# Optimization experiments

Hardware: AMD Instinct MI355X
Metric: run time of the kernel (lower is better)

The kernel has to match this reference:

```python
import jax, jax.numpy as jnp
import numpy as np

B, T, P, D = 8, 512, 2048, 768
TOKEN_HALF = 0.15
PATCH_HALF = 0.03  # small patch boxes


def _make_boxes(key, b, n, half):
    c = jax.random.uniform(key, (b, n, 2), dtype=jnp.float32)
    lo = jnp.clip(c - half, 0.0, 1.0)
    hi = jnp.clip(c + half, 0.0, 1.0)
    return jnp.concatenate([lo, hi], axis=-1)  # (b, n, 4): x0,y0,x1,y1


def setup_inputs() -> dict:
    key = jax.random.key(0)
    k1, k2, k3, k4 = jax.random.split(key, 4)
    patch_feats = jax.random.normal(k1, (B, P, D), dtype=jnp.float32)
    token_boxes = _make_boxes(k2, B, T, TOKEN_HALF)
    patch_boxes = _make_boxes(k3, B, P, PATCH_HALF)
    token_mask = jnp.ones((B, T), dtype=bool)
    scorer_w = jax.random.normal(k4, (D,), dtype=jnp.float32) * 0.02
    scorer_b = jnp.zeros((1,), dtype=jnp.float32)
    return {"patch_feats": patch_feats, "token_boxes": token_boxes,
            "patch_boxes": patch_boxes, "token_mask": token_mask,
            "scorer_w": scorer_w, "scorer_b": scorer_b}


def _patches_in_token_boxes(patch_boxes, tb):
    # patch center containment test: (B,T,P) bool
    cx = 0.5 * (patch_boxes[..., 0] + patch_boxes[..., 2])  # (B,P)
    cy = 0.5 * (patch_boxes[..., 1] + patch_boxes[..., 3])  # (B,P)
    cx = cx[:, None, :]
    cy = cy[:, None, :]
    return ((cx >= tb[..., 0:1]) & (cx <= tb[..., 2:3]) &
            (cy >= tb[..., 1:2]) & (cy <= tb[..., 3:4]))


def reference(patch_feats, token_boxes, patch_boxes, token_mask, scorer_w, scorer_b):
    # normalize token boxes if given in 0..1000 coords (data-dependent, via where)
    tb = token_boxes
    scale = jnp.where(tb.max() > 1.5, jnp.float32(1.0 / 1000.0), jnp.float32(1.0))
    tb = tb * scale

    in_box = _patches_in_token_boxes(patch_boxes, tb)          # (B,T,P)
    in_box = in_box & token_mask[:, :, None]
    region_mask = jnp.any(in_box, axis=-1)                      # (B,T)

    scores = patch_feats @ scorer_w + scorer_b[0]               # (B,P)
    scores = jnp.broadcast_to(scores[:, None, :], in_box.shape)  # (B,T,P)
    scores = jnp.where(in_box, scores, jnp.float32(-10000.0))
    attn = jax.nn.softmax(scores, axis=-1)                      # (B,T,P)

    region_feats = jnp.einsum('btp,bpd->btd', attn, patch_feats)
    region_feats = region_feats * region_mask[..., None].astype(region_feats.dtype)
    return region_feats, region_mask
```

## Files before the change

### kernel.cpp

```cpp
#include <hip/hip_runtime.h>

#define B 8
#define T 512
#define P 2048
#define D 768
#define KDIM P
#define NSPLIT 4
#define KSPLIT (KDIM / NSPLIT)

typedef unsigned short ushort_t;
using short8 = __attribute__((ext_vector_type(8))) short;
using f32x4v = __attribute__((ext_vector_type(4))) float;

#define IDX_SCALE 0
#define IDX_SCORES 64
#define IDX_SCORES2 (64 + B*P)
#define IDX_CX (64 + B*P)
#define IDX_CY (64 + 2*B*P)
#define OFF_ATTN_BYTES 197120
#define OFF_FT_BYTES (OFF_ATTN_BYTES + (size_t)B*T*P*2)
#define OFF_PART_BYTES (OFF_FT_BYTES + (size_t)B*D*P*2)
#define WS_NEED (OFF_PART_BYTES + (size_t)NSPLIT*B*T*D*4)

#define GLD16(gsrc, ldst) \
    __builtin_amdgcn_global_load_lds((const __attribute__((address_space(1))) void*)(gsrc), \
                                     (__attribute__((address_space(3))) void*)(ldst), 16, 0, 0)

__device__ inline ushort_t f2bf(float x) {
    union { float f; unsigned u; } v; v.f = x;
    unsigned r = v.u + 0x7fffu + ((v.u >> 16) & 1u);
    return (ushort_t)(r >> 16);
}

__global__ void k_scale(const float* __restrict__ tboxes, float* __restrict__ ws) {
    __shared__ float red[4];
    int tid = threadIdx.x;
    float m = -1e30f;
    const float4* tb4 = (const float4*)tboxes;
    #pragma unroll
    for (int i = 0; i < 16; ++i) {
        float4 v = tb4[tid + i * 256];
        m = fmaxf(fmaxf(fmaxf(m, v.x), fmaxf(v.y, v.z)), v.w);
    }
    #pragma unroll
    for (int off = 1; off < 64; off <<= 1) m = fmaxf(m, __shfl_xor(m, off));
    if ((tid & 63) == 0) red[tid >> 6] = m;
    __syncthreads();
    if (tid == 0) {
        float mb = fmaxf(fmaxf(red[0], red[1]), fmaxf(red[2], red[3]));
        ws[IDX_SCALE] = (mb > 1.5f) ? (1.0f / 1000.0f) : 1.0f;
    }
}

__global__ __launch_bounds__(256) void k_prep(const float* __restrict__ feats,
        const float* __restrict__ w, float* __restrict__ ws, ushort_t* __restrict__ fT) {
    __shared__ float tile[2][64][65];
    __shared__ float sred[64][17];
    const int t = threadIdx.x;
    const int p0 = blockIdx.x * 64;
    const int z = blockIdx.y;
    const int b = blockIdx.z;
    const float4* f4 = (const float4*)(feats + ((size_t)b * P + p0) * D);
    const float4* w4 = (const float4*)w;
    const int tr = t >> 4, tc = t & 15;
    float sp[4] = {0.f, 0.f, 0.f, 0.f};

    float4 v[4];
    {
        int dt = z * 6;
        #pragma unroll
        for (int i = 0; i < 4; ++i)
            v[i] = f4[(size_t)(tr + 16 * i) * 192 + dt * 16 + tc];
    }
    int cur = 0;
    for (int it = 0; it < 6; ++it) {
        const int dt = z * 6 + it;
        float4 wv = w4[dt * 16 + tc];
        #pragma unroll
        for (int i = 0; i < 4; ++i) {
            int pr = tr + 16 * i;
            sp[i] += v[i].x * wv.x + v[i].y * wv.y + v[i].z * wv.z + v[i].w * wv.w;
            tile[cur][pr][tc * 4 + 0] = v[i].x;
            tile[cur][pr][tc * 4 + 1] = v[i].y;
            tile[cur][pr][tc * 4 + 2] = v[i].z;
            tile[cur][pr][tc * 4 + 3] = v[i].w;
        }
        __syncthreads();
        if (it < 5) {
            int dt2 = dt + 1;
            #pragma unroll
            for (int i = 0; i < 4; ++i)
                v[i] = f4[(size_t)(tr + 16 * i) * 192 + dt2 * 16 + tc];
        }
        #pragma unroll
        for (int pass = 0; pass < 4; ++pass) {
            int idx = pass * 256 + t;
            int dr = idx >> 4;
            int pq = (idx & 15) * 4;
            unsigned u0 = (unsigned)f2bf(tile[cur][pq + 0][dr]) |
                          ((unsigned)f2bf(tile[cur][pq + 1][dr]) << 16);
            unsigned u1 = (unsigned)f2bf(tile[cur][pq + 2][dr]) |
                          ((unsigned)f2bf(tile[cur][pq + 3][dr]) << 16);
            uint2 o; o.x = u0; o.y = u1;
            *(uint2*)&fT[((size_t)b * D + dt * 64 + dr) * P + p0 + pq] = o;
        }
        cur ^= 1;
    }
    #pragma unroll
    for (int i = 0; i < 4; ++i) sred[tr + 16 * i][tc] = sp[i];
    __syncthreads();
    if (t < 64) {
        float s = 0.f;
        #pragma unroll
        for (int c = 0; c < 16; ++c) s += sred[t][c];
        ws[(z ? IDX_SCORES2 : IDX_SCORES) + b * P + p0 + t] = s;
    }
}

__global__ __launch_bounds__(256) void k_attn(const float* __restrict__ tboxes,
        const float* __restrict__ pboxes, const unsigned char* __restrict__ mask8,
        const float* __restrict__ bias, const float* __restrict__ ws,
        ushort_t* __restrict__ attn, float* __restrict__ out) {
    const int wv = threadIdx.x >> 6;
    const int ln = threadIdx.x & 63;
    const int t = blockIdx.x * 4 + wv;
    const int b = blockIdx.y;
    const int row = b * T + t;
    const float scale = ws[IDX_SCALE];
    const float bs = bias[0];
    const float4 tb = ((const float4*)tboxes)[row];
    const float lox = tb.x * scale, loy = tb.y * scale;
    const float hix = tb.z * scale, hiy = tb.w * scale;
    bool storage_u8 = ((mask8[1] | mask8[2] | mask8[3]) != 0);
    bool tmask = storage_u8 ? (mask8[row] != 0) : (((const int*)mask8)[row] != 0);

    const float2* sA = (const float2*)(ws + IDX_SCORES + b * P);
    const float2* sB = (const float2*)(ws + IDX_SCORES2 + b * P);
    const float4* pb4 = (const float4*)(pboxes + (size_t)b * P * 4);
    unsigned* arow32 = (unsigned*)(attn + (size_t)row * P);

    float s0[16], s1[16];
    float m = -1e30f;
    const float NINF = -__builtin_inff();
    #pragma unroll
    for (int r = 0; r < 16; ++r) {
        int q = ln + 64 * r;
        float2 sa = sA[q], sb = sB[q];
        float v0 = sa.x + sb.x + bs;
        float v1 = sa.y + sb.y + bs;
        float4 b0 = pb4[2 * q], b1 = pb4[2 * q + 1];
        float cx0 = 0.5f * (b0.x + b0.z), cy0 = 0.5f * (b0.y + b0.w);
        float cx1 = 0.5f * (b1.x + b1.z), cy1 = 0.5f * (b1.y + b1.w);
        bool i0 = (cx0 >= lox) && (cx0 <= hix) && (cy0 >= loy) && (cy0 <= hiy);
        bool i1 = (cx1 >= lox) && (cx1 <= hix) && (cy1 >= loy) && (cy1 <= hiy);
        s0[r] = i0 ? v0 : NINF;
        s1[r] = i1 ? v1 : NINF;
        m = fmaxf(m, fmaxf(s0[r], s1[r]));
    }
    #pragma unroll
    for (int off = 1; off < 64; off <<= 1) m = fmaxf(m, __shfl_xor(m, off));
    bool any = m > -1e29f;

    if (!any || !tmask) {
        #pragma unroll
        for (int r = 0; r < 16; ++r) arow32[ln + 64 * r] = 0u;
        if (ln == 0) out[(size_t)B * T * D + row] = 0.f;
        return;
    }
    float lsum = 0.f;
    #pragma unroll
    for (int r = 0; r < 16; ++r) {
        s0[r] = __expf(s0[r] - m);
        s1[r] = __expf(s1[r] - m);
        lsum += s0[r] + s1[r];
    }
    #pragma unroll
    for (int off = 1; off < 64; off <<= 1) lsum += __shfl_xor(lsum, off);
    float invl = 1.0f / lsum;
    #pragma unroll
    for (int r = 0; r < 16; ++r) {
        unsigned lo = (unsigned)f2bf(s0[r] * invl);
        unsigned hi = (unsigned)f2bf(s1[r] * invl);
        arow32[ln + 64 * r] = lo | (hi << 16);
    }
    if (ln == 0) out[(size_t)B * T * D + row] = 1.0f;
}

__global__ __launch_bounds__(256, 3) void k_gemm(const ushort_t* __restrict__ attn,
        const ushort_t* __restrict__ fT, float* __restrict__ partial) {
    __shared__ __align__(16) ushort_t As[8192];
    __shared__ __align__(16) ushort_t Bs[8192];
    const int tid = threadIdx.x;
    const int lane = tid & 63, wid = tid >> 6;
    const int wm = wid >> 1, wn = wid & 1;

    const int bid = blockIdx.x;
    const int b = bid & 7;
    const int w = bid >> 3;
    const int s = w / 24;
    const int tile = w % 24;
    const int t0 = (tile & 3) * 128;
    const int n0 = (tile >> 2) * 128;
    const int kbase = s * KSPLIT;

    const ushort_t* Ab = attn + ((size_t)b * T + t0) * P + kbase;
    const ushort_t* Bb = fT + ((size_t)b * D + n0) * P + kbase;

    const int rl8 = lane >> 3;
    const int slot = (lane & 7) ^ rl8;

    f32x4v acc[4][4];
    #pragma unroll
    for (int i = 0; i < 4; ++i)
        #pragma unroll
        for (int j = 0; j < 4; ++j)
            acc[i][j] = (f32x4v){0.f, 0.f, 0.f, 0.f};

    const int lr = lane & 15, hi4 = lane >> 4;

    #define LDA(row, kslot) (((row) >> 3) * 512 + ((row) & 7) * 64 + (((kslot) ^ ((row) & 7)) * 8))

    for (int kt = 0; kt < KSPLIT / 64; ++kt) {
        const ushort_t* a_src = Ab + (size_t)kt * 64;
        const ushort_t* b_src = Bb + (size_t)kt * 64;
        #pragma unroll
        for (int i = 0; i < 4; ++i) {
            int c = wid * 4 + i;
            GLD16(a_src + (size_t)(c * 8 + rl8) * P + slot * 8, &As[c * 512]);
        }
        #pragma unroll
        for (int i = 0; i < 4; ++i) {
            int c = wid * 4 + i;
            GLD16(b_src + (size_t)(c * 8 + rl8) * P + slot * 8, &Bs[c * 512]);
        }
        __syncthreads();
        #pragma unroll
        for (int ks = 0; ks < 2; ++ks) {
            short8 a[4], bfr[4];
            int kslot = ks * 4 + hi4;
            #pragma unroll
            for (int i = 0; i < 4; ++i)
                a[i] = *(const short8*)&As[LDA(wm * 64 + i * 16 + lr, kslot)];
            #pragma unroll
            for (int j = 0; j < 4; ++j)
                bfr[j] = *(const short8*)&Bs[LDA(wn * 64 + j * 16 + lr, kslot)];
            #pragma unroll
            for (int i = 0; i < 4; ++i)
                #pragma unroll
                for (int j = 0; j < 4; ++j)
                    acc[i][j] = __builtin_amdgcn_mfma_f32_16x16x32_bf16(a[i], bfr[j], acc[i][j], 0, 0, 0);
        }
        __syncthreads();
    }
    #undef LDA

    float* pout = partial + (size_t)s * B * T * D;
    #pragma unroll
    for (int i = 0; i < 4; ++i) {
        #pragma unroll
        for (int j = 0; j < 4; ++j) {
            int trow = t0 + wm * 64 + i * 16 + hi4 * 4;
            int ncol = n0 + wn * 64 + j * 16 + lr;
            #pragma unroll
            for (int q = 0; q < 4; ++q)
                pout[((size_t)(b * T) + trow + q) * D + ncol] = acc[i][j][q];
        }
    }
}

__global__ __launch_bounds__(256) void k_reduce(const float* __restrict__ partial,
                                                float* __restrict__ out) {
    const size_t i = (size_t)blockIdx.x * 256 + threadIdx.x;
    const size_t stride = (size_t)(B * T * D) / 4;
    const float4* p = (const float4*)partial;
    float4 a = p[i], b2 = p[i + stride], c = p[i + 2 * stride], d = p[i + 3 * stride];
    float4 r;
    r.x = ((a.x + b2.x) + c.x) + d.x;
    r.y = ((a.y + b2.y) + c.y) + d.y;
    r.z = ((a.z + b2.z) + c.z) + d.z;
    r.w = ((a.w + b2.w) + c.w) + d.w;
    ((float4*)out)[i] = r;
}

__global__ __launch_bounds__(256) void k_scores_fb(
        const float* __restrict__ feats, const float* __restrict__ pboxes,
        const float* __restrict__ w, const float* __restrict__ bias,
        float* __restrict__ ws) {
    int row = blockIdx.x * 4 + (threadIdx.x >> 6);
    int lane = threadIdx.x & 63;
    const float* f = feats + (size_t)row * D;
    float acc = 0.f;
    #pragma unroll
    for (int k = 0; k < D / 64; ++k) acc += f[lane + k * 64] * w[lane + k * 64];
    #pragma unroll
    for (int off = 1; off < 64; off <<= 1) acc += __shfl_xor(acc, off);
    if (lane == 0) {
        ws[IDX_SCORES + row] = acc + bias[0];
        ws[IDX_CX + row] = 0.5f * (pboxes[row * 4 + 0] + pboxes[row * 4 + 2]);
        ws[IDX_CY + row] = 0.5f * (pboxes[row * 4 + 1] + pboxes[row * 4 + 3]);
    }
}

__global__ __launch_bounds__(256) void k_main_fb(
        const float* __restrict__ feats, const float* __restrict__ tboxes,
        const unsigned char* __restrict__ mask8,
        const float* __restrict__ ws, float* __restrict__ out) {
    const int t = blockIdx.x, b = blockIdx.y;
    const int tid = threadIdx.x;
    const float scale = ws[IDX_SCALE];
    const float* scores = ws + IDX_SCORES;
    const float* cxs = ws + IDX_CX;
    const float* cys = ws + IDX_CY;
    const int row = b * T + t;
    const float lo_x = tboxes[row * 4 + 0] * scale;
    const float lo_y = tboxes[row * 4 + 1] * scale;
    const float hi_x = tboxes[row * 4 + 2] * scale;
    const float hi_y = tboxes[row * 4 + 3] * scale;
    bool storage_u8 = ((mask8[1] | mask8[2] | mask8[3]) != 0);
    bool tmask = storage_u8 ? (mask8[row] != 0) : (((const int*)mask8)[row] != 0);
    float s[8]; bool ib[8];
    float m = -1e30f;
    #pragma unroll
    for (int j = 0; j < 8; ++j) {
        int p = tid + j * 256;
        float cx = cxs[b * P + p], cy = cys[b * P + p];
        bool in = (cx >= lo_x) && (cx <= hi_x) && (cy >= lo_y) && (cy <= hi_y);
        ib[j] = in;
        s[j] = scores[b * P + p];
        if (in) m = fmaxf(m, s[j]);
    }
    __shared__ float s_red[4];
    #pragma unroll
    for (int off = 1; off < 64; off <<= 1) m = fmaxf(m, __shfl_xor(m, off));
    if ((tid & 63) == 0) s_red[tid >> 6] = m;
    __syncthreads();
    float mb = fmaxf(fmaxf(s_red[0], s_red[1]), fmaxf(s_red[2], s_red[3]));
    bool any = mb > -1e29f;
    const size_t obase = (size_t)row * D;
    if (!any || !tmask) {
        out[obase + tid] = 0.f; out[obase + tid + 256] = 0.f; out[obase + tid + 512] = 0.f;
        if (tid == 0) out[(size_t)B * T * D + row] = 0.f;
        return;
    }
    float w8[8]; int c = 0; float lsum = 0.f;
    #pragma unroll
    for (int j = 0; j < 8; ++j) {
        float wv = ib[j] ? __expf(s[j] - mb) : 0.f;
        w8[j] = wv; lsum += wv;
        if (ib[j]) ++c;
    }
    __shared__ float s_sum[4];
    #pragma unroll
    for (int off = 1; off < 64; off <<= 1) lsum += __shfl_xor(lsum, off);
    if ((tid & 63) == 0) s_sum[tid >> 6] = lsum;
    __syncthreads();
    float l = s_sum[0] + s_sum[1] + s_sum[2] + s_sum[3];
    __shared__ int s_cnt[256];
    s_cnt[tid] = c;
    __syncthreads();
    #pragma unroll
    for (int off = 1; off < 256; off <<= 1) {
        int v = (tid >= off) ? s_cnt[tid - off] : 0;
        __syncthreads();
        s_cnt[tid] += v;
        __syncthreads();
    }
    int excl = s_cnt[tid] - c;
    int nnz = s_cnt[255];
    __shared__ int s_idx[P];
    __shared__ float s_wt[P];
    int o = excl;
    #pragma unroll
    for (int j = 0; j < 8; ++j) {
        if (ib[j]) { s_idx[o] = tid + j * 256; s_wt[o] = w8[j]; ++o; }
    }
    __syncthreads();
    float a0 = 0.f, a1 = 0.f, a2 = 0.f;
    const float* fb = feats + (size_t)b * P * D;
    for (int i = 0; i < nnz; ++i) {
        int p = s_idx[i];
        float wv = s_wt[i];
        const float* fr = fb + (size_t)p * D + tid;
        a0 += wv * fr[0]; a1 += wv * fr[256]; a2 += wv * fr[512];
    }
    float inv = 1.0f / l;
    out[obase + tid] = a0 * inv;
    out[obase + tid + 256] = a1 * inv;
    out[obase + tid + 512] = a2 * inv;
    if (tid == 0) out[(size_t)B * T * D + row] = 1.0f;
}

extern "C" void kernel_launch(void* const* d_in, const int* in_sizes, int n_in,
                              void* d_out, int out_size, void* d_ws, size_t ws_size,
                              hipStream_t stream) {
    const float* feats  = (const float*)d_in[0];
    const float* tboxes = (const float*)d_in[1];
    const float* pboxes = (const float*)d_in[2];
    const unsigned char* tmask = (const unsigned char*)d_in[3];
    const float* w      = (const float*)d_in[4];
    const float* bias   = (const float*)d_in[5];
    float* out = (float*)d_out;
    float* ws  = (float*)d_ws;

    if (ws_size >= WS_NEED) {
        ushort_t* attn = (ushort_t*)((char*)d_ws + OFF_ATTN_BYTES);
        ushort_t* fT   = (ushort_t*)((char*)d_ws + OFF_FT_BYTES);
        float* part    = (float*)((char*)d_ws + OFF_PART_BYTES);
        k_scale<<<1, 256, 0, stream>>>(tboxes, ws);
        k_prep<<<dim3(P / 64, 2, B), 256, 0, stream>>>(feats, w, ws, fT);
        k_attn<<<dim3(T / 4, B), 256, 0, stream>>>(tboxes, pboxes, tmask, bias, ws, attn, out);
        k_gemm<<<dim3(NSPLIT * B * (T / 128) * (D / 128)), 256, 0, stream>>>(attn, fT, part);
        k_reduce<<<dim3(B * T * D / 4 / 256), 256, 0, stream>>>(part, out);
    } else {
        k_scale<<<1, 256, 0, stream>>>(tboxes, ws);
        k_scores_fb<<<(B * P) / 4, 256, 0, stream>>>(feats, pboxes, w, bias, ws);
        k_main_fb<<<dim3(T, B), 256, 0, stream>>>(feats, tboxes, tmask, ws, out);
    }
}
```

Baseline: 62.66 us.

## Replace dense attention matrix with bitmask and per-patch exp scores in GEMM

Instead of materialising the bf16 (B,T,P) softmax matrix, this computes exp(score) once per patch and a per-token containment bitmask. The GEMM rebuilds its A operand in registers by masking the exp values with the bitmask, and the reduce step applies the 1/sum normalisation. The split-K factor drops from 4 to 2, which halves the partial buffer traffic. Skipping max subtraction risks overflow or underflow for large scores and changes rounding, and the GEMM now has half as many blocks.

```diff
diff --git a/kernel.cpp b/kernel.cpp
--- a/kernel.cpp
+++ b/kernel.cpp
@@ -5,10 +5,11 @@
 #define P 2048
 #define D 768
 #define KDIM P
-#define NSPLIT 4
+#define NSPLIT 2
 #define KSPLIT (KDIM / NSPLIT)
 
 typedef unsigned short ushort_t;
+typedef unsigned long long u64_t;
 using short8 = __attribute__((ext_vector_type(8))) short;
 using f32x4v = __attribute__((ext_vector_type(4))) float;
 
@@ -18,6 +19,9 @@
 #define IDX_CX (64 + B*P)
 #define IDX_CY (64 + 2*B*P)
 #define OFF_ATTN_BYTES 197120
+#define OFF_MASK_BYTES OFF_ATTN_BYTES
+#define OFF_EINV_BYTES (OFF_MASK_BYTES + (size_t)B*T*32*8)
+#define OFF_ES16_BYTES (OFF_EINV_BYTES + (size_t)B*T*4)
 #define OFF_FT_BYTES (OFF_ATTN_BYTES + (size_t)B*T*P*2)
 #define OFF_PART_BYTES (OFF_FT_BYTES + (size_t)B*D*P*2)
 #define WS_NEED (OFF_PART_BYTES + (size_t)NSPLIT*B*T*D*4)
@@ -117,78 +121,66 @@
     }
 }
 
-__global__ __launch_bounds__(256) void k_attn(const float* __restrict__ tboxes,
+__global__ __launch_bounds__(256) void k_es(const float* __restrict__ ws,
+        const float* __restrict__ bias, unsigned* __restrict__ es16) {
+    int i = blockIdx.x * 256 + threadIdx.x;
+    float2 sa = ((const float2*)(ws + IDX_SCORES))[i];
+    float2 sb = ((const float2*)(ws + IDX_SCORES2))[i];
+    float bs = bias[0];
+    unsigned lo = (unsigned)f2bf(__expf(sa.x + sb.x + bs));
+    unsigned hi = (unsigned)f2bf(__expf(sa.y + sb.y + bs));
+    es16[i] = lo | (hi << 16);
+}
+
+__global__ __launch_bounds__(256) void k_stats(const float* __restrict__ tboxes,
         const float* __restrict__ pboxes, const unsigned char* __restrict__ mask8,
-        const float* __restrict__ bias, const float* __restrict__ ws,
-        ushort_t* __restrict__ attn, float* __restrict__ out) {
+        const float* __restrict__ ws, const unsigned* __restrict__ es16,
+        u64_t* __restrict__ mask64, float* __restrict__ einv, float* __restrict__ out) {
     const int wv = threadIdx.x >> 6;
     const int ln = threadIdx.x & 63;
     const int t = blockIdx.x * 4 + wv;
     const int b = blockIdx.y;
     const int row = b * T + t;
     const float scale = ws[IDX_SCALE];
-    const float bs = bias[0];
     const float4 tb = ((const float4*)tboxes)[row];
     const float lox = tb.x * scale, loy = tb.y * scale;
     const float hix = tb.z * scale, hiy = tb.w * scale;
     bool storage_u8 = ((mask8[1] | mask8[2] | mask8[3]) != 0);
     bool tmask = storage_u8 ? (mask8[row] != 0) : (((const int*)mask8)[row] != 0);
 
-    const float2* sA = (const float2*)(ws + IDX_SCORES + b * P);
-    const float2* sB = (const float2*)(ws + IDX_SCORES2 + b * P);
     const float4* pb4 = (const float4*)(pboxes + (size_t)b * P * 4);
-    unsigned* arow32 = (unsigned*)(attn + (size_t)row * P);
-
-    float s0[16], s1[16];
-    float m = -1e30f;
-    const float NINF = -__builtin_inff();
-    #pragma unroll
-    for (int r = 0; r < 16; ++r) {
-        int q = ln + 64 * r;
-        float2 sa = sA[q], sb = sB[q];
-        float v0 = sa.x + sb.x + bs;
-        float v1 = sa.y + sb.y + bs;
-        float4 b0 = pb4[2 * q], b1 = pb4[2 * q + 1];
-        float cx0 = 0.5f * (b0.x + b0.z), cy0 = 0.5f * (b0.y + b0.w);
-        float cx1 = 0.5f * (b1.x + b1.z), cy1 = 0.5f * (b1.y + b1.w);
-        bool i0 = (cx0 >= lox) && (cx0 <= hix) && (cy0 >= loy) && (cy0 <= hiy);
-        bool i1 = (cx1 >= lox) && (cx1 <= hix) && (cy1 >= loy) && (cy1 <= hiy);
-        s0[r] = i0 ? v0 : NINF;
-        s1[r] = i1 ? v1 : NINF;
-        m = fmaxf(m, fmaxf(s0[r], s1[r]));
-    }
-    #pragma unroll
-    for (int off = 1; off < 64; off <<= 1) m = fmaxf(m, __shfl_xor(m, off));
-    bool any = m > -1e29f;
-
-    if (!any || !tmask) {
-        #pragma unroll
-        for (int r = 0; r < 16; ++r) arow32[ln + 64 * r] = 0u;
-        if (ln == 0) out[(size_t)B * T * D + row] = 0.f;
-        return;
-    }
+    const unsigned* esb = es16 + (size_t)b * P / 2;
+    const int par = ln & 1;
+    const int halfln = ln >> 1;
+
+    u64_t myword = 0;
     float lsum = 0.f;
     #pragma unroll
-    for (int r = 0; r < 16; ++r) {
-        s0[r] = __expf(s0[r] - m);
-        s1[r] = __expf(s1[r] - m);
-        lsum += s0[r] + s1[r];
+    for (int r = 0; r < 32; ++r) {
+        int p = ln + 64 * r;
+        float4 bx = pb4[p];
+        float cx = 0.5f * (bx.x + bx.z);
+        float cy = 0.5f * (bx.y + bx.w);
+        bool in = (cx >= lox) && (cx <= hix) && (cy >= loy) && (cy <= hiy);
+        unsigned pr = esb[halfln + 32 * r];
+        float e = __uint_as_float(par ? (pr & 0xffff0000u) : (pr << 16));
+        lsum += in ? e : 0.f;
+        u64_t w = __ballot(in);
+        if (r == ln) myword = w;
     }
     #pragma unroll
     for (int off = 1; off < 64; off <<= 1) lsum += __shfl_xor(lsum, off);
-    float invl = 1.0f / lsum;
-    #pragma unroll
-    for (int r = 0; r < 16; ++r) {
-        unsigned lo = (unsigned)f2bf(s0[r] * invl);
-        unsigned hi = (unsigned)f2bf(s1[r] * invl);
-        arow32[ln + 64 * r] = lo | (hi << 16);
-    }
-    if (ln == 0) out[(size_t)B * T * D + row] = 1.0f;
-}
-
-__global__ __launch_bounds__(256, 3) void k_gemm(const ushort_t* __restrict__ attn,
-        const ushort_t* __restrict__ fT, float* __restrict__ partial) {
-    __shared__ __align__(16) ushort_t As[8192];
+    bool live = (lsum > 0.f) && tmask;
+    if (ln < 32) mask64[(size_t)row * 32 + ln] = myword;
+    if (ln == 0) {
+        einv[row] = live ? (1.0f / lsum) : 0.f;
+        out[(size_t)B * T * D + row] = live ? 1.f : 0.f;
+    }
+}
+
+__global__ __launch_bounds__(256, 3) void k_gemm(const unsigned* __restrict__ es16,
+        const u64_t* __restrict__ mask64, const ushort_t* __restrict__ fT,
+        float* __restrict__ partial) {
     __shared__ __align__(16) ushort_t Bs[8192];
     const int tid = threadIdx.x;
     const int lane = tid & 63, wid = tid >> 6;
@@ -196,18 +188,22 @@
 
     const int bid = blockIdx.x;
     const int b = bid & 7;
-    const int w = bid >> 3;
-    const int s = w / 24;
-    const int tile = w % 24;
+    const int rem = bid >> 3;
+    const int s = (rem >= 24) ? 1 : 0;
+    const int tile = (rem >= 24) ? rem - 24 : rem;
     const int t0 = (tile & 3) * 128;
     const int n0 = (tile >> 2) * 128;
     const int kbase = s * KSPLIT;
 
-    const ushort_t* Ab = attn + ((size_t)b * T + t0) * P + kbase;
     const ushort_t* Bb = fT + ((size_t)b * D + n0) * P + kbase;
 
     const int rl8 = lane >> 3;
     const int slot = (lane & 7) ^ rl8;
+    const int lr = lane & 15, hi4 = lane >> 4;
+    const int shift = hi4 * 8;
+
+    const u64_t* mbase = mask64 + (size_t)(b * T + t0 + wm * 64 + lr) * 32 + s * 16;
+    const uint4* es4 = (const uint4*)(es16 + (size_t)(b * P + kbase) / 2);
 
     f32x4v acc[4][4];
     #pragma unroll
@@ -216,43 +212,50 @@
         for (int j = 0; j < 4; ++j)
             acc[i][j] = (f32x4v){0.f, 0.f, 0.f, 0.f};
 
-    const int lr = lane & 15, hi4 = lane >> 4;
-
-    #define LDA(row, kslot) (((row) >> 3) * 512 + ((row) & 7) * 64 + (((kslot) ^ ((row) & 7)) * 8))
+    #define LDB(row, kslot) (((row) >> 3) * 512 + ((row) & 7) * 64 + (((kslot) ^ ((row) & 7)) * 8))
 
     for (int kt = 0; kt < KSPLIT / 64; ++kt) {
-        const ushort_t* a_src = Ab + (size_t)kt * 64;
-        const ushort_t* b_src = Bb + (size_t)kt * 64;
         #pragma unroll
         for (int i = 0; i < 4; ++i) {
             int c = wid * 4 + i;
-            GLD16(a_src + (size_t)(c * 8 + rl8) * P + slot * 8, &As[c * 512]);
-        }
-        #pragma unroll
-        for (int i = 0; i < 4; ++i) {
-            int c = wid * 4 + i;
-            GLD16(b_src + (size_t)(c * 8 + rl8) * P + slot * 8, &Bs[c * 512]);
-        }
+            GLD16(Bb + (size_t)(c * 8 + rl8) * P + kt * 64 + slot * 8, &Bs[c * 512]);
+        }
+        u64_t wv0 = mbase[0 * 512 + kt];
+        u64_t wv1 = mbase[1 * 512 + kt];
+        u64_t wv2 = mbase[2 * 512 + kt];
+        u64_t wv3 = mbase[3 * 512 + kt];
+        uint4 ep0 = es4[kt * 8 + hi4];
+        uint4 ep1 = es4[kt * 8 + 4 + hi4];
         __syncthreads();
         #pragma unroll
         for (int ks = 0; ks < 2; ++ks) {
-            short8 a[4], bfr[4];
+            const unsigned q0 = ks ? ep1.x : ep0.x;
+            const unsigned q1 = ks ? ep1.y : ep0.y;
+            const unsigned q2 = ks ? ep1.z : ep0.z;
+            const unsigned q3 = ks ? ep1.w : ep0.w;
             int kslot = ks * 4 + hi4;
-            #pragma unroll
-            for (int i = 0; i < 4; ++i)
-                a[i] = *(const short8*)&As[LDA(wm * 64 + i * 16 + lr, kslot)];
+            short8 bfr[4];
             #pragma unroll
             for (int j = 0; j < 4; ++j)
-                bfr[j] = *(const short8*)&Bs[LDA(wn * 64 + j * 16 + lr, kslot)];
+                bfr[j] = *(const short8*)&Bs[LDB(wn * 64 + j * 16 + lr, kslot)];
             #pragma unroll
-            for (int i = 0; i < 4; ++i)
+            for (int i = 0; i < 4; ++i) {
+                u64_t wvi = (i == 0) ? wv0 : (i == 1) ? wv1 : (i == 2) ? wv2 : wv3;
+                unsigned half = ks ? (unsigned)(wvi >> 32) : (unsigned)wvi;
+                unsigned byte = (half >> shift) & 0xffu;
+                union { short8 s8; unsigned u[4]; } au;
+                au.u[0] = q0 & (((byte & 1u)   ? 0xffffu : 0u) | ((byte & 2u)   ? 0xffff0000u : 0u));
+                au.u[1] = q1 & (((byte & 4u)   ? 0xffffu : 0u) | ((byte & 8u)   ? 0xffff0000u : 0u));
+                au.u[2] = q2 & (((byte & 16u)  ? 0xffffu : 0u) | ((byte & 32u)  ? 0xffff0000u : 0u));
+                au.u[3] = q3 & (((byte & 64u)  ? 0xffffu : 0u) | ((byte & 128u) ? 0xffff0000u : 0u));
                 #pragma unroll
                 for (int j = 0; j < 4; ++j)
-                    acc[i][j] = __builtin_amdgcn_mfma_f32_16x16x32_bf16(a[i], bfr[j], acc[i][j], 0, 0, 0);
+                    acc[i][j] = __builtin_amdgcn_mfma_f32_16x16x32_bf16(au.s8, bfr[j], acc[i][j], 0, 0, 0);
+            }
         }
         __syncthreads();
     }
-    #undef LDA
+    #undef LDB
 
     float* pout = partial + (size_t)s * B * T * D;
     #pragma unroll
@@ -269,16 +272,18 @@
 }
 
 __global__ __launch_bounds__(256) void k_reduce(const float* __restrict__ partial,
-                                                float* __restrict__ out) {
+        const float* __restrict__ einv, float* __restrict__ out) {
     const size_t i = (size_t)blockIdx.x * 256 + threadIdx.x;
     const size_t stride = (size_t)(B * T * D) / 4;
     const float4* p = (const float4*)partial;
-    float4 a = p[i], b2 = p[i + stride], c = p[i + 2 * stride], d = p[i + 3 * stride];
+    float4 a = p[i], b2 = p[i + stride];
+    int row = (int)((i * 4) / D);
+    float e = einv[row];
     float4 r;
-    r.x = ((a.x + b2.x) + c.x) + d.x;
-    r.y = ((a.y + b2.y) + c.y) + d.y;
-    r.z = ((a.z + b2.z) + c.z) + d.z;
-    r.w = ((a.w + b2.w) + c.w) + d.w;
+    r.x = (a.x + b2.x) * e;
+    r.y = (a.y + b2.y) * e;
+    r.z = (a.z + b2.z) * e;
+    r.w = (a.w + b2.w) * e;
     ((float4*)out)[i] = r;
 }
 
@@ -403,14 +408,17 @@
     float* ws  = (float*)d_ws;
 
     if (ws_size >= WS_NEED) {
-        ushort_t* attn = (ushort_t*)((char*)d_ws + OFF_ATTN_BYTES);
+        u64_t* mask64  = (u64_t*)((char*)d_ws + OFF_MASK_BYTES);
+        float* einv    = (float*)((char*)d_ws + OFF_EINV_BYTES);
+        unsigned* es16 = (unsigned*)((char*)d_ws + OFF_ES16_BYTES);
         ushort_t* fT   = (ushort_t*)((char*)d_ws + OFF_FT_BYTES);
         float* part    = (float*)((char*)d_ws + OFF_PART_BYTES);
         k_scale<<<1, 256, 0, stream>>>(tboxes, ws);
         k_prep<<<dim3(P / 64, 2, B), 256, 0, stream>>>(feats, w, ws, fT);
-        k_attn<<<dim3(T / 4, B), 256, 0, stream>>>(tboxes, pboxes, tmask, bias, ws, attn, out);
-        k_gemm<<<dim3(NSPLIT * B * (T / 128) * (D / 128)), 256, 0, stream>>>(attn, fT, part);
-        k_reduce<<<dim3(B * T * D / 4 / 256), 256, 0, stream>>>(part, out);
+        k_es<<<dim3(B * P / 2 / 256), 256, 0, stream>>>(ws, bias, es16);
+        k_stats<<<dim3(T / 4, B), 256, 0, stream>>>(tboxes, pboxes, tmask, ws, es16, mask64, einv, out);
+        k_gemm<<<dim3(NSPLIT * B * (T / 128) * (D / 128)), 256, 0, stream>>>(es16, mask64, fT, part);
+        k_reduce<<<dim3(B * T * D / 4 / 256), 256, 0, stream>>>(part, einv, out);
     } else {
         k_scale<<<1, 256, 0, stream>>>(tboxes, ws);
         k_scores_fb<<<(B * P) / 4, 256, 0, stream>>>(feats, pboxes, w, bias, ws);
```

After: 72.25 us. 1.15x slower.
